# Kernel optimization log

Measured on AMD Instinct MI355X. Metric: run time of the kernel, lower is better.

The kernel has to match this reference:

```python
import jax, jax.numpy as jnp
import numpy as np

N_NODES = 100000


def gcn_conv(h, edge_index, W, b):
    """PyG GCNConv: add self-loops, symmetric normalization, linear transform,
    sum aggregation over incoming edges, plus bias."""
    n = h.shape[0]
    loop = jnp.arange(n)
    row = jnp.concatenate([edge_index[0], loop])  # source nodes
    col = jnp.concatenate([edge_index[1], loop])  # destination nodes
    # degree of destination nodes (edge weight = 1)
    deg = jax.ops.segment_sum(jnp.ones_like(col, dtype=h.dtype), col, num_segments=n)
    dinv = jnp.where(deg > 0, jax.lax.rsqrt(deg), 0.0)
    norm = dinv[row] * dinv[col]  # [E+n]
    hW = h @ W                    # [n, out] small GEMM
    msg = hW[row] * norm[:, None] # gather + scale, [E+n, out]
    out = jax.ops.segment_sum(msg, col, num_segments=n)  # scatter-add
    return out + b


def setup_inputs() -> dict:
    key = jax.random.key(0)
    k1, k2, k3, k4 = jax.random.split(key, 4)
    N, E, D_IN, D_H, D_OUT = N_NODES, 1600000, 64, 64, 32
    x = jax.random.normal(k1, (N, D_IN), dtype=jnp.float32)
    edge_index = jax.random.randint(k2, (2, E), 0, N, dtype=jnp.int64)
    W1 = jax.random.normal(k3, (D_IN, D_H), dtype=jnp.float32) / np.sqrt(D_IN)
    b1 = jnp.zeros((D_H,), dtype=jnp.float32)
    W2 = jax.random.normal(k4, (D_H, D_OUT), dtype=jnp.float32) / np.sqrt(D_H)
    b2 = jnp.zeros((D_OUT,), dtype=jnp.float32)
    return {"x": x, "edge_index": edge_index, "W1": W1, "b1": b1, "W2": W2, "b2": b2}


def reference(x, edge_index, W1, b1, W2, b2):
    # StackedGCNEncoder.encode, eval mode (dropout is identity at inference)
    h = gcn_conv(x, edge_index, W1, b1)
    h = jax.nn.relu(h)
    h = gcn_conv(h, edge_index, W2, b2)
    return h
```

## Files before the change

kernel.cpp:

```cpp
#include <hip/hip_runtime.h>

#define NN 100000
#define NNr 100016
#define NE 1600000
#define STRIDE 48
#define PSZ 12500
#define NCH 1563
#define SEGCAP 256
#define NSB 49
#define CAP2 160

static __device__ __forceinline__ unsigned short f2bf(float f) {
    unsigned int u = __float_as_uint(f);
    return (unsigned short)((u + 0x7FFFu + ((u >> 16) & 1u)) >> 16);
}
static __device__ __forceinline__ float bflo(unsigned int u) {
    return __uint_as_float(u << 16);
}
static __device__ __forceinline__ float bfhi(unsigned int u) {
    return __uint_as_float(u & 0xFFFF0000u);
}
static __device__ __forceinline__ unsigned int bfpack(float lo, float hi) {
    return ((unsigned int)f2bf(lo)) | (((unsigned int)f2bf(hi)) << 16);
}

__global__ __launch_bounds__(256, 6) void fused1_k(const float* __restrict__ x,
        const float* __restrict__ W1, unsigned short* __restrict__ A,
        const int* __restrict__ ei, int2* __restrict__ segs,
        int* __restrict__ segcnt) {
    __shared__ __align__(16) char smem_raw[25088];
    __shared__ int bcnt[8];

    const int bid = blockIdx.x;
    if (bid % 3 == 0) {
        int2* bins = reinterpret_cast<int2*>(smem_raw);
        const int c = bid / 3;
        if (threadIdx.x < 8) bcnt[threadIdx.x] = 0;
        __syncthreads();

        long long base = (long long)c * 1024 + (long long)threadIdx.x * 4;
        if (base < NE) {
            int4 s = *reinterpret_cast<const int4*>(ei + base);
            int4 d = *reinterpret_cast<const int4*>(ei + NE + base);
            int p0 = d.x / PSZ, p1 = d.y / PSZ, p2 = d.z / PSZ, p3 = d.w / PSZ;
            int q0 = atomicAdd(&bcnt[p0], 1);
            if (q0 < SEGCAP) bins[p0 * SEGCAP + q0] = make_int2(s.x, d.x);
            int q1 = atomicAdd(&bcnt[p1], 1);
            if (q1 < SEGCAP) bins[p1 * SEGCAP + q1] = make_int2(s.y, d.y);
            int q2 = atomicAdd(&bcnt[p2], 1);
            if (q2 < SEGCAP) bins[p2 * SEGCAP + q2] = make_int2(s.z, d.z);
            int q3 = atomicAdd(&bcnt[p3], 1);
            if (q3 < SEGCAP) bins[p3 * SEGCAP + q3] = make_int2(s.w, d.w);
        }
        __syncthreads();

#pragma unroll 1
        for (int p = 0; p < 8; ++p) {
            int n = min(bcnt[p], SEGCAP);
            long long sbase = ((long long)p * NCH + c) * SEGCAP;
            for (int i = threadIdx.x; i < n; i += 256) segs[sbase + i] = bins[p * SEGCAP + i];
            if (threadIdx.x == 0) segcnt[p * NCH + c] = n;
        }
        return;
    }

    const int gemmIdx = (bid % 3 == 1) ? 2 * (bid / 3) : 2 * (bid / 3) + 1;
    if (gemmIdx >= 3125) return;
    const int row0 = gemmIdx * 32;

    float* sH = reinterpret_cast<float*>(smem_raw);
    float* sW = reinterpret_cast<float*>(smem_raw) + 32 * 68;

    for (int i = threadIdx.x; i < 16 * 64; i += 256)
        *reinterpret_cast<float4*>(&sW[i * 4]) = reinterpret_cast<const float4*>(W1)[i];
    for (int t = threadIdx.x; t < 32 * 16; t += 256) {
        int r = t >> 4, k4 = (t & 15) << 2;
        *reinterpret_cast<float4*>(&sH[r * 68 + k4]) =
            *reinterpret_cast<const float4*>(x + (long long)(row0 + r) * 64 + k4);
    }
    __syncthreads();

    const int tc = threadIdx.x & 15, tr = threadIdx.x >> 4;
    const int rb = tr * 2, cb = tc * 4;
    float acc[2][4] = {};
#pragma unroll
    for (int k = 0; k < 64; k += 4) {
        float a[2][4], w[4][4];
#pragma unroll
        for (int i = 0; i < 2; ++i) {
            float4 t4 = *reinterpret_cast<const float4*>(&sH[(rb + i) * 68 + k]);
            a[i][0] = t4.x; a[i][1] = t4.y; a[i][2] = t4.z; a[i][3] = t4.w;
        }
#pragma unroll
        for (int kk = 0; kk < 4; ++kk) {
            float4 t4 = *reinterpret_cast<const float4*>(&sW[(k + kk) * 64 + cb]);
            w[kk][0] = t4.x; w[kk][1] = t4.y; w[kk][2] = t4.z; w[kk][3] = t4.w;
        }
#pragma unroll
        for (int i = 0; i < 2; ++i)
#pragma unroll
            for (int kk = 0; kk < 4; ++kk)
#pragma unroll
                for (int j = 0; j < 4; ++j)
                    acc[i][j] = fmaf(a[i][kk], w[kk][j], acc[i][j]);
    }
#pragma unroll
    for (int i = 0; i < 2; ++i) {
        ushort4 o;
        o.x = f2bf(acc[i][0]); o.y = f2bf(acc[i][1]);
        o.z = f2bf(acc[i][2]); o.w = f2bf(acc[i][3]);
        *reinterpret_cast<ushort4*>(A + (long long)(row0 + rb + i) * 64 + cb) = o;
    }
}

__global__ __launch_bounds__(256) void bin2_k(const int2* __restrict__ segs,
        const int* __restrict__ segcnt, int2* __restrict__ segs2,
        int* __restrict__ seg2cnt) {
    __shared__ int lc[NSB];
    const int p = blockIdx.x / NSB, kb = blockIdx.x % NSB;
    const int plo = p * PSZ;
    if (threadIdx.x < NSB) lc[threadIdx.x] = 0;
    __syncthreads();

    const long long obase = (long long)blockIdx.x * NSB * CAP2;
#pragma unroll 1
    for (int c = kb; c < NCH; c += NSB) {
        int n = segcnt[p * NCH + c];
        long long sbase = ((long long)p * NCH + c) * SEGCAP;
        for (int i = threadIdx.x; i < n; i += 256) {
            int2 e = segs[sbase + i];
            int sb = (e.y - plo) >> 8;
            int r = atomicAdd(&lc[sb], 1);
            if (r < CAP2) segs2[obase + (long long)sb * CAP2 + r] = e;
        }
    }
    __syncthreads();
    if (threadIdx.x < NSB)
        seg2cnt[blockIdx.x * NSB + threadIdx.x] = min(lc[threadIdx.x], CAP2);
}

__global__ __launch_bounds__(256) void build_k(const int2* __restrict__ segs2,
        const int* __restrict__ seg2cnt, int* __restrict__ cursor,
        int* __restrict__ csr, unsigned int* __restrict__ A32) {
    __shared__ int lc[256];
    __shared__ int lcsr[256 * STRIDE];
    const int p = blockIdx.x / NSB, sb = blockIdx.x % NSB;
    const int vb = p * PSZ + sb * 256;
    const int nloc = min(256, PSZ - sb * 256);
    lc[threadIdx.x] = 0;
    __syncthreads();

#pragma unroll 1
    for (int kb = 0; kb < NSB; ++kb) {
        const int bix = p * NSB + kb;
        int n = seg2cnt[bix * NSB + sb];
        long long sbase = ((long long)bix * NSB + sb) * CAP2;
        for (int i = threadIdx.x; i < n; i += 256) {
            int2 e = segs2[sbase + i];
            int l = e.y - vb;
            int slot = atomicAdd(&lc[l], 1);
            if (slot < STRIDE) lcsr[l * STRIDE + slot] = e.x;
        }
    }
    __syncthreads();

    if (threadIdx.x < nloc) cursor[vb + threadIdx.x] = lc[threadIdx.x];
    for (int t = threadIdx.x; t < nloc * STRIDE; t += 256)
        csr[(long long)vb * STRIDE + t] = lcsr[t];

    for (int t = threadIdx.x; t < nloc * 8; t += 256) {
        int l = t >> 3, c = t & 7;
        float di = rsqrtf((float)lc[l] + 1.0f);
        uint4 u = reinterpret_cast<uint4*>(A32)[(long long)(vb + l) * 8 + c];
        u.x = bfpack(bflo(u.x) * di, bfhi(u.x) * di);
        u.y = bfpack(bflo(u.y) * di, bfhi(u.y) * di);
        u.z = bfpack(bflo(u.z) * di, bfhi(u.z) * di);
        u.w = bfpack(bflo(u.w) * di, bfhi(u.w) * di);
        reinterpret_cast<uint4*>(A32)[(long long)(vb + l) * 8 + c] = u;
    }
}

__global__ __launch_bounds__(256) void gather_gemm2_k(const int* __restrict__ cursor,
        const int* __restrict__ csr, const uint2* __restrict__ A64,
        const float* __restrict__ b1, const float* __restrict__ W2,
        unsigned short* __restrict__ C, int n) {
    __shared__ __align__(16) float sW2[64 * 32];
    __shared__ float sB[4][64];

    for (int i = threadIdx.x; i < 16 * 32; i += 256)
        *reinterpret_cast<float4*>(&sW2[i * 4]) = reinterpret_cast<const float4*>(W2)[i];
    __syncthreads();

    const int wv = threadIdx.x >> 6, lane = threadIdx.x & 63;
    const int q = lane >> 4;
    const int fl = lane & 15;
    const int v = blockIdx.x * 4 + wv;
    if (v >= n) return;

    const int cv = cursor[v];
    const int deg = min(cv, STRIDE);
    const float dv = rsqrtf((float)cv + 1.0f);

    int rl = 0;
    if (lane < deg) rl = csr[v * STRIDE + lane];

    const uint2 av = A64[(unsigned)(v * 16 + fl)];

    float m0 = 0.f, m1 = 0.f, m2 = 0.f, m3 = 0.f;
    const uint2 z = make_uint2(0u, 0u);
    const int T = (deg + 15) >> 4;
    for (int it = 0; it < T; ++it) {
        const int e0 = it * 16 + q;
        int r0 = __shfl(rl, e0);
        int r1 = __shfl(rl, e0 + 4);
        int r2 = __shfl(rl, e0 + 8);
        int r3 = __shfl(rl, e0 + 12);
        uint2 a0 = (e0      < deg) ? A64[(unsigned)(r0 * 16 + fl)] : z;
        uint2 a1 = (e0 + 4  < deg) ? A64[(unsigned)(r1 * 16 + fl)] : z;
        uint2 a2 = (e0 + 8  < deg) ? A64[(unsigned)(r2 * 16 + fl)] : z;
        uint2 a3 = (e0 + 12 < deg) ? A64[(unsigned)(r3 * 16 + fl)] : z;
        m0 += bflo(a0.x); m1 += bfhi(a0.x); m2 += bflo(a0.y); m3 += bfhi(a0.y);
        m0 += bflo(a1.x); m1 += bfhi(a1.x); m2 += bflo(a1.y); m3 += bfhi(a1.y);
        m0 += bflo(a2.x); m1 += bfhi(a2.x); m2 += bflo(a2.y); m3 += bfhi(a2.y);
        m0 += bflo(a3.x); m1 += bfhi(a3.x); m2 += bflo(a3.y); m3 += bfhi(a3.y);
    }
    m0 += __shfl_xor(m0, 16); m0 += __shfl_xor(m0, 32);
    m1 += __shfl_xor(m1, 16); m1 += __shfl_xor(m1, 32);
    m2 += __shfl_xor(m2, 16); m2 += __shfl_xor(m2, 32);
    m3 += __shfl_xor(m3, 16); m3 += __shfl_xor(m3, 32);

    if (q == 0) {
        float4 bb = reinterpret_cast<const float4*>(b1)[fl];
        float4 o;
        o.x = fmaxf(fmaf(dv, m0 + bflo(av.x), bb.x), 0.0f);
        o.y = fmaxf(fmaf(dv, m1 + bfhi(av.x), bb.y), 0.0f);
        o.z = fmaxf(fmaf(dv, m2 + bflo(av.y), bb.z), 0.0f);
        o.w = fmaxf(fmaf(dv, m3 + bfhi(av.y), bb.w), 0.0f);
        *reinterpret_cast<float4*>(&sB[wv][4 * fl]) = o;
    }
    __builtin_amdgcn_wave_barrier();

    const int j = lane & 31, kbase = (lane >> 5) << 5;
    float pj = 0.0f;
#pragma unroll
    for (int t = 0; t < 32; ++t) {
        int k = kbase + t;
        pj = fmaf(sB[wv][k], sW2[k * 32 + j], pj);
    }
    pj += __shfl_down(pj, 32);
    if (lane < 32) C[(long long)v * 32 + j] = f2bf(pj * dv);
}

__global__ __launch_bounds__(256) void gather2_k(const int* __restrict__ cursor,
        const int* __restrict__ csr, const uint2* __restrict__ C64,
        const float* __restrict__ b2, float* __restrict__ outp, int n) {
    const int wv = threadIdx.x >> 6, lane = threadIdx.x & 63;
    const int q = lane >> 3;
    const int fl = lane & 7;
    const int v = blockIdx.x * 4 + wv;
    if (v >= n) return;

    const int cv = cursor[v];
    const int deg = min(cv, STRIDE);
    const float dv = rsqrtf((float)cv + 1.0f);

    int rl = 0;
    if (lane < deg) rl = csr[v * STRIDE + lane];

    const uint2 cvu = C64[(unsigned)(v * 8 + fl)];

    float m0 = 0.f, m1 = 0.f, m2 = 0.f, m3 = 0.f;
    const uint2 z = make_uint2(0u, 0u);
    const int T = (deg + 31) >> 5;
    for (int it = 0; it < T; ++it) {
        const int e0 = it * 32 + q;
        int r0 = __shfl(rl, e0);
        int r1 = __shfl(rl, e0 + 8);
        int r2 = __shfl(rl, e0 + 16);
        int r3 = __shfl(rl, e0 + 24);
        uint2 c0 = (e0      < deg) ? C64[(unsigned)(r0 * 8 + fl)] : z;
        uint2 c1 = (e0 + 8  < deg) ? C64[(unsigned)(r1 * 8 + fl)] : z;
        uint2 c2 = (e0 + 16 < deg) ? C64[(unsigned)(r2 * 8 + fl)] : z;
        uint2 c3 = (e0 + 24 < deg) ? C64[(unsigned)(r3 * 8 + fl)] : z;
        m0 += bflo(c0.x); m1 += bfhi(c0.x); m2 += bflo(c0.y); m3 += bfhi(c0.y);
        m0 += bflo(c1.x); m1 += bfhi(c1.x); m2 += bflo(c1.y); m3 += bfhi(c1.y);
        m0 += bflo(c2.x); m1 += bfhi(c2.x); m2 += bflo(c2.y); m3 += bfhi(c2.y);
        m0 += bflo(c3.x); m1 += bfhi(c3.x); m2 += bflo(c3.y); m3 += bfhi(c3.y);
    }
    m0 += __shfl_xor(m0, 8); m0 += __shfl_xor(m0, 16); m0 += __shfl_xor(m0, 32);
    m1 += __shfl_xor(m1, 8); m1 += __shfl_xor(m1, 16); m1 += __shfl_xor(m1, 32);
    m2 += __shfl_xor(m2, 8); m2 += __shfl_xor(m2, 16); m2 += __shfl_xor(m2, 32);
    m3 += __shfl_xor(m3, 8); m3 += __shfl_xor(m3, 16); m3 += __shfl_xor(m3, 32);

    if (q == 0) {
        float4 bb = reinterpret_cast<const float4*>(b2)[fl];
        float4 o;
        o.x = fmaf(dv, m0 + bflo(cvu.x), bb.x);
        o.y = fmaf(dv, m1 + bfhi(cvu.x), bb.y);
        o.z = fmaf(dv, m2 + bflo(cvu.y), bb.z);
        o.w = fmaf(dv, m3 + bfhi(cvu.y), bb.w);
        reinterpret_cast<float4*>(outp)[(unsigned)(v * 8 + fl)] = o;
    }
}

extern "C" void kernel_launch(void* const* d_in, const int* in_sizes, int n_in,
                              void* d_out, int out_size, void* d_ws, size_t ws_size,
                              hipStream_t stream) {
    const float* x  = (const float*)d_in[0];
    const int*   ei = (const int*)d_in[1];
    const float* W1 = (const float*)d_in[2];
    const float* b1 = (const float*)d_in[3];
    const float* W2 = (const float*)d_in[4];
    const float* b2 = (const float*)d_in[5];
    float* out = (float*)d_out;

    char* base = (char*)d_ws;
    unsigned short* A       = (unsigned short*)base;
    int*            segcnt  = (int*)(base + 12800000);
    long long off_R1  = 12800000 + 50176;
    int2*           segs    = (int2*)(base + off_R1);
    int*            cursor  = (int*)(base + off_R1);
    int*            csr     = cursor + NNr;
    long long off_s2c = off_R1 + 25608192;
    int*            seg2cnt = (int*)(base + off_s2c);
    long long off_R2  = off_s2c + 77056;
    int2*           segs2   = (int2*)(base + off_R2);
    unsigned short* C       = (unsigned short*)(base + off_R2);

    const int BT = 256;

    fused1_k<<<4689, BT, 0, stream>>>(x, W1, A, ei, segs, segcnt);
    bin2_k<<<392, BT, 0, stream>>>(segs, segcnt, segs2, seg2cnt);
    build_k<<<392, BT, 0, stream>>>(segs2, seg2cnt, cursor, csr, (unsigned int*)A);
    gather_gemm2_k<<<(NN + 3) / 4, BT, 0, stream>>>(cursor, csr,
        (const uint2*)A, b1, W2, C, NN);
    gather2_k<<<(NN + 3) / 4, BT, 0, stream>>>(cursor, csr,
        (const uint2*)C, b2, out, NN);
}
```

Measured before the change: 157.6 us.

## Split layer-1 gather from second GEMM into separate tiled GEMM kernel

The fused gather+GEMM kernel is split in two. gather1_k now writes the ReLU'd hidden layer to a bf16 buffer. A new register-tiled gemm2_k then multiplies 128-row tiles by W2 from shared memory and applies the degree scaling. This drops the per-wave W2 load into LDS and the scalar per-lane GEMM from the gather kernel, in exchange for an extra kernel launch and a 12.8 MB round trip through memory plus bf16 rounding of the hidden layer.

```diff
diff --git a/kernel.cpp b/kernel.cpp
--- a/kernel.cpp
+++ b/kernel.cpp
@@ -180,17 +180,9 @@
     }
 }
 
-__global__ __launch_bounds__(256) void gather_gemm2_k(const int* __restrict__ cursor,
+__global__ __launch_bounds__(256) void gather1_k(const int* __restrict__ cursor,
         const int* __restrict__ csr, const uint2* __restrict__ A64,
-        const float* __restrict__ b1, const float* __restrict__ W2,
-        unsigned short* __restrict__ C, int n) {
-    __shared__ __align__(16) float sW2[64 * 32];
-    __shared__ float sB[4][64];
-
-    for (int i = threadIdx.x; i < 16 * 32; i += 256)
-        *reinterpret_cast<float4*>(&sW2[i * 4]) = reinterpret_cast<const float4*>(W2)[i];
-    __syncthreads();
-
+        const float* __restrict__ b1, uint2* __restrict__ B64, int n) {
     const int wv = threadIdx.x >> 6, lane = threadIdx.x & 63;
     const int q = lane >> 4;
     const int fl = lane & 15;
@@ -231,24 +223,74 @@
 
     if (q == 0) {
         float4 bb = reinterpret_cast<const float4*>(b1)[fl];
-        float4 o;
-        o.x = fmaxf(fmaf(dv, m0 + bflo(av.x), bb.x), 0.0f);
-        o.y = fmaxf(fmaf(dv, m1 + bfhi(av.x), bb.y), 0.0f);
-        o.z = fmaxf(fmaf(dv, m2 + bflo(av.y), bb.z), 0.0f);
-        o.w = fmaxf(fmaf(dv, m3 + bfhi(av.y), bb.w), 0.0f);
-        *reinterpret_cast<float4*>(&sB[wv][4 * fl]) = o;
-    }
-    __builtin_amdgcn_wave_barrier();
-
-    const int j = lane & 31, kbase = (lane >> 5) << 5;
-    float pj = 0.0f;
-#pragma unroll
-    for (int t = 0; t < 32; ++t) {
-        int k = kbase + t;
-        pj = fmaf(sB[wv][k], sW2[k * 32 + j], pj);
-    }
-    pj += __shfl_down(pj, 32);
-    if (lane < 32) C[(long long)v * 32 + j] = f2bf(pj * dv);
+        float B0 = fmaxf(fmaf(dv, m0 + bflo(av.x), bb.x), 0.0f);
+        float B1 = fmaxf(fmaf(dv, m1 + bfhi(av.x), bb.y), 0.0f);
+        float B2 = fmaxf(fmaf(dv, m2 + bflo(av.y), bb.z), 0.0f);
+        float B3 = fmaxf(fmaf(dv, m3 + bfhi(av.y), bb.w), 0.0f);
+        uint2 o;
+        o.x = bfpack(B0, B1);
+        o.y = bfpack(B2, B3);
+        B64[(unsigned)(v * 16 + fl)] = o;
+    }
+}
+
+__global__ __launch_bounds__(256) void gemm2_k(const uint4* __restrict__ B32,
+        const float* __restrict__ W2, const int* __restrict__ cursor,
+        unsigned short* __restrict__ C, int n) {
+    __shared__ __align__(16) float sH[128 * 68];
+    __shared__ __align__(16) float sW[64 * 32];
+
+    const int row0 = blockIdx.x * 128;
+
+    for (int i = threadIdx.x; i < 512; i += 256)
+        reinterpret_cast<float4*>(sW)[i] = reinterpret_cast<const float4*>(W2)[i];
+    for (int t = threadIdx.x; t < 1024; t += 256) {
+        int r = t >> 3, g = t & 7;
+        int gr = min(row0 + r, n - 1);
+        uint4 u = B32[(unsigned)(gr * 8 + g)];
+        float4 lo, hi;
+        lo.x = bflo(u.x); lo.y = bfhi(u.x); lo.z = bflo(u.y); lo.w = bfhi(u.y);
+        hi.x = bflo(u.z); hi.y = bfhi(u.z); hi.z = bflo(u.w); hi.w = bfhi(u.w);
+        *reinterpret_cast<float4*>(&sH[r * 68 + g * 8]) = lo;
+        *reinterpret_cast<float4*>(&sH[r * 68 + g * 8 + 4]) = hi;
+    }
+    __syncthreads();
+
+    const int tc = threadIdx.x & 7, tr = threadIdx.x >> 3;
+    const int cb = tc * 4;
+    float acc[4][4] = {};
+#pragma unroll
+    for (int k = 0; k < 64; k += 4) {
+        float a[4][4], w[4][4];
+#pragma unroll
+        for (int i = 0; i < 4; ++i) {
+            float4 t4 = *reinterpret_cast<const float4*>(&sH[(tr + 32 * i) * 68 + k]);
+            a[i][0] = t4.x; a[i][1] = t4.y; a[i][2] = t4.z; a[i][3] = t4.w;
+        }
+#pragma unroll
+        for (int kk = 0; kk < 4; ++kk) {
+            float4 t4 = *reinterpret_cast<const float4*>(&sW[(k + kk) * 32 + cb]);
+            w[kk][0] = t4.x; w[kk][1] = t4.y; w[kk][2] = t4.z; w[kk][3] = t4.w;
+        }
+#pragma unroll
+        for (int i = 0; i < 4; ++i)
+#pragma unroll
+            for (int kk = 0; kk < 4; ++kk)
+#pragma unroll
+                for (int j = 0; j < 4; ++j)
+                    acc[i][j] = fmaf(a[i][kk], w[kk][j], acc[i][j]);
+    }
+#pragma unroll
+    for (int i = 0; i < 4; ++i) {
+        int gr = row0 + tr + 32 * i;
+        if (gr < n) {
+            float dvr = rsqrtf((float)cursor[gr] + 1.0f);
+            ushort4 o;
+            o.x = f2bf(acc[i][0] * dvr); o.y = f2bf(acc[i][1] * dvr);
+            o.z = f2bf(acc[i][2] * dvr); o.w = f2bf(acc[i][3] * dvr);
+            *reinterpret_cast<ushort4*>(&C[(long long)gr * 32 + cb]) = o;
+        }
+    }
 }
 
 __global__ __launch_bounds__(256) void gather2_k(const int* __restrict__ cursor,
@@ -326,14 +368,16 @@
     long long off_R2  = off_s2c + 77056;
     int2*           segs2   = (int2*)(base + off_R2);
     unsigned short* C       = (unsigned short*)(base + off_R2);
+    unsigned short* B       = (unsigned short*)(base + off_R2 + 6400000);
 
     const int BT = 256;
 
     fused1_k<<<4689, BT, 0, stream>>>(x, W1, A, ei, segs, segcnt);
     bin2_k<<<392, BT, 0, stream>>>(segs, segcnt, segs2, seg2cnt);
     build_k<<<392, BT, 0, stream>>>(segs2, seg2cnt, cursor, csr, (unsigned int*)A);
-    gather_gemm2_k<<<(NN + 3) / 4, BT, 0, stream>>>(cursor, csr,
-        (const uint2*)A, b1, W2, C, NN);
+    gather1_k<<<(NN + 3) / 4, BT, 0, stream>>>(cursor, csr,
+        (const uint2*)A, b1, (uint2*)B, NN);
+    gemm2_k<<<(NN + 127) / 128, BT, 0, stream>>>((const uint4*)B, W2, cursor, C, NN);
     gather2_k<<<(NN + 3) / 4, BT, 0, stream>>>(cursor, csr,
         (const uint2*)C, b2, out, NN);
 }
```

Result: slower. 171.9 us (+9.0%).
